# Optimization experiments

Hardware: AMD Instinct MI355X
Metric: run time of the kernel (lower is better)

The kernel has to match this reference:

```python
import jax, jax.numpy as jnp
import numpy as np
import math

B, N, E, D = 8, 2048, 2048, 128
MAX_K = 8
HYPER_DIM = 128
LN_EPS = 1e-5


def _sinusoidal_pe(max_pos, dim):
    pe = np.zeros((max_pos, dim), dtype=np.float32)
    position = np.arange(max_pos, dtype=np.float32)[:, None]
    div_term = np.exp(np.arange(0, dim, 2, dtype=np.float32) * (-math.log(10000.0) / dim))
    pe[:, 0::2] = np.sin(position * div_term)
    pe[:, 1::2] = np.cos(position * div_term)
    return jnp.asarray(pe)


def setup_inputs() -> dict:
    key = jax.random.key(0)
    ks = jax.random.split(key, 24)
    s = 0.05
    inp = {
        'x_v': jax.random.normal(ks[0], (B, N, D), jnp.float32),
        'x_e': jax.random.normal(ks[1], (B, E, D), jnp.float32),
        'incidence': (jax.random.uniform(ks[2], (B, N, E), jnp.float32) < 0.01).astype(jnp.float32),
        'suffix_normalizer': jax.random.uniform(ks[3], (B, N), jnp.float32) * 20.0,
        'edge_orders': 1 + jax.random.randint(ks[4], (B, E), 0, MAX_K),
        'node_mask': jax.random.randint(ks[5], (B, N), 0, 2) > 0,
        'edge_mask': jax.random.randint(ks[6], (B, E), 0, 2) > 0,
        'pe1_table': _sinusoidal_pe(MAX_K + 1, D),
        'pe2_table': _sinusoidal_pe(2, D),
        'bias_b': jax.random.uniform(ks[7], (1, D), jnp.float32, -1, 1) / math.sqrt(D),
    }
    i = 8
    for m in ('mlp1', 'mlp2', 'mlp3'):
        inp[m + '_W1'] = jax.random.normal(ks[i], (D, HYPER_DIM), jnp.float32) * s; i += 1
        inp[m + '_b1'] = jnp.zeros((HYPER_DIM,), jnp.float32)
        inp[m + '_W2'] = jax.random.normal(ks[i], (HYPER_DIM, D), jnp.float32) * s; i += 1
        inp[m + '_b2'] = jnp.zeros((D,), jnp.float32)
    for n in ('norm1', 'norm2', 'norm3'):
        inp[n + '_g'] = jnp.ones((D,), jnp.float32)
        inp[n + '_b'] = jnp.zeros((D,), jnp.float32)
    return inp


def _ln(x, g, b):
    mu = jnp.mean(x, axis=-1, keepdims=True)
    var = jnp.mean(jnp.square(x - mu), axis=-1, keepdims=True)
    return (x - mu) * jax.lax.rsqrt(var + LN_EPS) * g + b


def _mlp(x, W1, b1, W2, b2):
    return jax.nn.relu(x @ W1 + b1) @ W2 + b2


def reference(x_v, x_e, incidence, suffix_normalizer, edge_orders, node_mask, edge_mask,
              pe1_table, pe2_table, bias_b,
              mlp1_W1, mlp1_b1, mlp1_W2, mlp1_b2,
              mlp2_W1, mlp2_b1, mlp2_W2, mlp2_b2,
              mlp3_W1, mlp3_b1, mlp3_W2, mlp3_b2,
              norm1_g, norm1_b, norm2_g, norm2_b, norm3_g, norm3_b):
    nm = node_mask[..., None]  # [B,N,1]
    em = edge_mask[..., None]  # [B,E,1]
    x_v = jnp.where(nm, x_v, 0.0)
    x_e = jnp.where(em, x_e, 0.0)
    pe1_k1 = pe1_table[1][None, None, :]          # [1,1,D]
    pe1_k = pe1_table[edge_orders]                # [B,E,D]
    x_v = x_v + _mlp(_ln(x_v, norm1_g, norm1_b) + pe1_k1, mlp1_W1, mlp1_b1, mlp1_W2, mlp1_b2)
    x_e = x_e + _mlp(_ln(x_e, norm1_g, norm1_b) + pe1_k, mlp1_W1, mlp1_b1, mlp1_W2, mlp1_b2)
    x_v = jnp.where(nm, x_v, 0.0)
    x_e = jnp.where(em, x_e, 0.0)
    agg = jnp.einsum('bne,bed->bnd', incidence, x_e)
    x1 = x_v + agg / (1.0 + suffix_normalizer[..., None])
    pe2_s1 = pe2_table[1][None, None, :]
    x1 = x1 + _mlp(_ln(x1, norm2_g, norm2_b) + pe2_s1, mlp2_W1, mlp2_b1, mlp2_W2, mlp2_b2)
    x = jnp.where(nm, x1, 0.0)
    x = x + _mlp(_ln(x, norm3_g, norm3_b), mlp3_W1, mlp3_b1, mlp3_W2, mlp3_b2)
    x = x + bias_b
    x = jnp.where(nm, x, 0.0)
    return x
```

## Files before the change

### kernel.cpp

```cpp
#include <hip/hip_runtime.h>
#include <stdint.h>

#define BB 8
#define NN 2048
#define EE 2048
#define DD 128
#define RBP 132
#define NTHREADS 256
#define WMAT_U32 8192
#define LCAP 64

typedef __attribute__((ext_vector_type(8))) short bf16x8;
typedef __attribute__((ext_vector_type(4))) float f32x4;

__device__ inline unsigned bf16rne(float f) {
    unsigned u = __float_as_uint(f);
    return (u + 0x7fffu + ((u >> 16) & 1u)) >> 16;
}
__device__ inline float bf16lo(unsigned u) { return __uint_as_float(u << 16); }
__device__ inline float bf16hi(unsigned u) { return __uint_as_float(u & 0xffff0000u); }

#define SWZ(b) ((b) ^ ((((b) >> 8) & 7) << 4))

struct __align__(16) SmemK1 {
    float rowbuf[32][RBP];
    unsigned h[32 * 64];
    int rmask[32];
    int ords[32];
};

struct __align__(16) SmemK3 {
    float rowbuf[16][RBP];
    unsigned h[16 * 64];
    int rmask[16];
};

__device__ inline void load_rows32(SmemK1& s, const float* __restrict__ src) {
    int t = threadIdx.x;
    for (int idx = t; idx < 32 * 32; idx += NTHREADS) {
        int r = idx >> 5, c4 = (idx & 31) * 4;
        float4 v = *(const float4*)&src[r * DD + c4];
        *(float4*)&s.rowbuf[r][c4] = v;
    }
    __syncthreads();
    for (int idx = t; idx < 32 * 32; idx += NTHREADS) {
        int r = idx >> 5, c4 = (idx & 31) * 4;
        if (s.rmask[r] == 0) *(float4*)&s.rowbuf[r][c4] = make_float4(0.f, 0.f, 0.f, 0.f);
    }
    __syncthreads();
}

__device__ inline void ln32(SmemK1& s, const float* __restrict__ gw,
                            const float* __restrict__ bw,
                            const float* __restrict__ pe_base, bool per_row_pe) {
    int t = threadIdx.x;
    int gr = t >> 3, g = t & 7;
    int base = g * 16;
    float x[16];
    float4* xp = (float4*)x;
    xp[0] = *(const float4*)&s.rowbuf[gr][base + 0];
    xp[1] = *(const float4*)&s.rowbuf[gr][base + 4];
    xp[2] = *(const float4*)&s.rowbuf[gr][base + 8];
    xp[3] = *(const float4*)&s.rowbuf[gr][base + 12];
    float s1 = 0.f, s2 = 0.f;
    #pragma unroll
    for (int i = 0; i < 16; i++) { s1 += x[i]; s2 += x[i] * x[i]; }
    #pragma unroll
    for (int off = 1; off < 8; off <<= 1) {
        s1 += __shfl_xor(s1, off, 64);
        s2 += __shfl_xor(s2, off, 64);
    }
    float mu = s1 * (1.f / 128.f);
    float var = s2 * (1.f / 128.f) - mu * mu;
    float rstd = rsqrtf(var + 1e-5f);
    const float* pe = nullptr;
    if (pe_base) pe = per_row_pe ? (pe_base + (size_t)s.ords[gr] * DD) : pe_base;
    unsigned p[8];
    #pragma unroll
    for (int j = 0; j < 8; j++) {
        int k0 = base + 2 * j;
        float v0 = (x[2 * j] - mu) * rstd * gw[k0] + bw[k0];
        float v1 = (x[2 * j + 1] - mu) * rstd * gw[k0 + 1] + bw[k0 + 1];
        if (pe) { v0 += pe[k0]; v1 += pe[k0 + 1]; }
        p[j] = bf16rne(v0) | (bf16rne(v1) << 16);
    }
    char* hb = (char*)s.h;
    int byte0 = gr * 256 + g * 32;
    uint4 lo = make_uint4(p[0], p[1], p[2], p[3]);
    uint4 hi = make_uint4(p[4], p[5], p[6], p[7]);
    *(uint4*)(hb + SWZ(byte0)) = lo;
    *(uint4*)(hb + SWZ(byte0 + 16)) = hi;
    __syncthreads();
}

template <bool TO_H>
__device__ inline void mm32_f32w(SmemK1& s, const float* __restrict__ Wf,
                                 const float* __restrict__ bias) {
    int t = threadIdx.x;
    int w = t >> 6, l = t & 63;
    int lm = l & 15, lk = l >> 4;
    bf16x8 bfr[2][4];
    #pragma unroll
    for (int nbl = 0; nbl < 2; nbl++) {
        int n = w * 32 + nbl * 16 + lm;
        #pragma unroll
        for (int kb = 0; kb < 4; kb++) {
            int k0 = kb * 32 + lk * 8;
            unsigned pk[4];
            #pragma unroll
            for (int jp = 0; jp < 4; jp++) {
                float a = Wf[(size_t)(k0 + 2 * jp) * DD + n];
                float b = Wf[(size_t)(k0 + 2 * jp + 1) * DD + n];
                pk[jp] = bf16rne(a) | (bf16rne(b) << 16);
            }
            uint4 u = make_uint4(pk[0], pk[1], pk[2], pk[3]);
            bfr[nbl][kb] = *(bf16x8*)&u;
        }
    }
    const char* hb = (const char*)s.h;
    bf16x8 afr[2][4];
    #pragma unroll
    for (int mb = 0; mb < 2; mb++) {
        int row = mb * 16 + lm;
        #pragma unroll
        for (int kb = 0; kb < 4; kb++)
            afr[mb][kb] = *(const bf16x8*)(hb + SWZ(row * 256 + kb * 64 + lk * 16));
    }
    f32x4 acc[2][2];
    #pragma unroll
    for (int mb = 0; mb < 2; mb++)
        #pragma unroll
        for (int nbl = 0; nbl < 2; nbl++)
            acc[mb][nbl] = (f32x4){0.f, 0.f, 0.f, 0.f};
    #pragma unroll
    for (int kb = 0; kb < 4; kb++)
        #pragma unroll
        for (int mb = 0; mb < 2; mb++)
            #pragma unroll
            for (int nbl = 0; nbl < 2; nbl++)
                acc[mb][nbl] = __builtin_amdgcn_mfma_f32_16x16x32_bf16(
                    afr[mb][kb], bfr[nbl][kb], acc[mb][nbl], 0, 0, 0);
    float bcol0 = bias[w * 32 + lm];
    float bcol1 = bias[w * 32 + 16 + lm];
    __syncthreads();
    if (TO_H) {
        char* hw = (char*)s.h;
        #pragma unroll
        for (int mb = 0; mb < 2; mb++)
            #pragma unroll
            for (int nbl = 0; nbl < 2; nbl++) {
                int col = w * 32 + nbl * 16 + lm;
                float bc = nbl ? bcol1 : bcol0;
                #pragma unroll
                for (int j = 0; j < 4; j++) {
                    int row = mb * 16 + lk * 4 + j;
                    float v = fmaxf(acc[mb][nbl][j] + bc, 0.f);
                    *(unsigned short*)(hw + SWZ(row * 256 + col * 2)) =
                        (unsigned short)bf16rne(v);
                }
            }
    } else {
        #pragma unroll
        for (int mb = 0; mb < 2; mb++)
            #pragma unroll
            for (int nbl = 0; nbl < 2; nbl++) {
                int col = w * 32 + nbl * 16 + lm;
                float bc = nbl ? bcol1 : bcol0;
                #pragma unroll
                for (int j = 0; j < 4; j++) {
                    int row = mb * 16 + lk * 4 + j;
                    s.rowbuf[row][col] += acc[mb][nbl][j] + bc;
                }
            }
    }
    __syncthreads();
}

__device__ inline void ln16(SmemK3& s, const float* __restrict__ gw,
                            const float* __restrict__ bw,
                            const float* __restrict__ pe) {
    int t = threadIdx.x;
    int gr = t >> 4, g = t & 15;
    int base = g * 8;
    float x[8];
    float4* xp = (float4*)x;
    xp[0] = *(const float4*)&s.rowbuf[gr][base + 0];
    xp[1] = *(const float4*)&s.rowbuf[gr][base + 4];
    float s1 = 0.f, s2 = 0.f;
    #pragma unroll
    for (int i = 0; i < 8; i++) { s1 += x[i]; s2 += x[i] * x[i]; }
    #pragma unroll
    for (int off = 1; off < 16; off <<= 1) {
        s1 += __shfl_xor(s1, off, 64);
        s2 += __shfl_xor(s2, off, 64);
    }
    float mu = s1 * (1.f / 128.f);
    float var = s2 * (1.f / 128.f) - mu * mu;
    float rstd = rsqrtf(var + 1e-5f);
    unsigned p[4];
    #pragma unroll
    for (int j = 0; j < 4; j++) {
        int k0 = base + 2 * j;
        float v0 = (x[2 * j] - mu) * rstd * gw[k0] + bw[k0];
        float v1 = (x[2 * j + 1] - mu) * rstd * gw[k0 + 1] + bw[k0 + 1];
        if (pe) { v0 += pe[k0]; v1 += pe[k0 + 1]; }
        p[j] = bf16rne(v0) | (bf16rne(v1) << 16);
    }
    char* hb = (char*)s.h;
    uint4 q = make_uint4(p[0], p[1], p[2], p[3]);
    *(uint4*)(hb + SWZ(gr * 256 + g * 16)) = q;
    __syncthreads();
}

template <bool TO_H>
__device__ inline void mm16(SmemK3& s, const unsigned* __restrict__ WT,
                            const float* __restrict__ bias) {
    int t = threadIdx.x;
    int w = t >> 6, l = t & 63;
    int lm = l & 15, lk = l >> 4;
    bf16x8 bfr[2][4];
    const uint4* wt4 = (const uint4*)WT;
    #pragma unroll
    for (int nbl = 0; nbl < 2; nbl++) {
        int n = w * 32 + nbl * 16 + lm;
        #pragma unroll
        for (int kb = 0; kb < 4; kb++) {
            uint4 u = wt4[n * 16 + kb * 4 + lk];
            bfr[nbl][kb] = *(bf16x8*)&u;
        }
    }
    const char* hb = (const char*)s.h;
    bf16x8 afr[4];
    #pragma unroll
    for (int kb = 0; kb < 4; kb++)
        afr[kb] = *(const bf16x8*)(hb + SWZ(lm * 256 + kb * 64 + lk * 16));
    f32x4 acc[2];
    acc[0] = (f32x4){0.f, 0.f, 0.f, 0.f};
    acc[1] = (f32x4){0.f, 0.f, 0.f, 0.f};
    #pragma unroll
    for (int kb = 0; kb < 4; kb++)
        #pragma unroll
        for (int nbl = 0; nbl < 2; nbl++)
            acc[nbl] = __builtin_amdgcn_mfma_f32_16x16x32_bf16(
                afr[kb], bfr[nbl][kb], acc[nbl], 0, 0, 0);
    float bcol0 = bias[w * 32 + lm];
    float bcol1 = bias[w * 32 + 16 + lm];
    __syncthreads();
    if (TO_H) {
        char* hw = (char*)s.h;
        #pragma unroll
        for (int nbl = 0; nbl < 2; nbl++) {
            int col = w * 32 + nbl * 16 + lm;
            float bc = nbl ? bcol1 : bcol0;
            #pragma unroll
            for (int j = 0; j < 4; j++) {
                int row = lk * 4 + j;
                float v = fmaxf(acc[nbl][j] + bc, 0.f);
                *(unsigned short*)(hw + SWZ(row * 256 + col * 2)) =
                    (unsigned short)bf16rne(v);
            }
        }
    } else {
        #pragma unroll
        for (int nbl = 0; nbl < 2; nbl++) {
            int col = w * 32 + nbl * 16 + lm;
            float bc = nbl ? bcol1 : bcol0;
            #pragma unroll
            for (int j = 0; j < 4; j++) {
                int row = lk * 4 + j;
                s.rowbuf[row][col] += acc[nbl][j] + bc;
            }
        }
    }
    __syncthreads();
}

__global__ __launch_bounds__(NTHREADS) void k1_kernel(
    const float* __restrict__ x_e, const float* __restrict__ x_v,
    const int* __restrict__ emask, const int* __restrict__ nmask,
    const int* __restrict__ eord, const float* __restrict__ pe1,
    const float* __restrict__ n1g, const float* __restrict__ n1b,
    const float* __restrict__ W11, const float* __restrict__ b11,
    const float* __restrict__ W12, const float* __restrict__ b12,
    const float* __restrict__ W21, const float* __restrict__ W22,
    const float* __restrict__ W31, const float* __restrict__ W32,
    unsigned* __restrict__ WT, unsigned* __restrict__ e2pk,
    float* __restrict__ v2out) {
    __shared__ SmemK1 s;
    int bid = blockIdx.x;
    int t = threadIdx.x;
    int gtid = bid * NTHREADS + t;
    if (gtid < 4 * WMAT_U32) {
        int mat = gtid >> 13;
        int idx = gtid & (WMAT_U32 - 1);
        int n = idx >> 6, j = idx & 63;
        const float* W = mat == 0 ? W21 : mat == 1 ? W22 : mat == 2 ? W31 : W32;
        float a = W[(2 * j) * DD + n];
        float b = W[(2 * j + 1) * DD + n];
        WT[gtid] = bf16rne(a) | (bf16rne(b) << 16);
    }
    bool isEdge = bid < (BB * EE / 32);
    int mb = isEdge ? bid : bid - (BB * EE / 32);
    int bb = mb & 7;
    int r0 = (mb >> 3) * 32;
    int rowbase = bb * EE + r0;
    const int* mask = isEdge ? emask : nmask;
    if (t < 32) {
        s.rmask[t] = mask[rowbase + t];
        if (isEdge) {
            int o = eord[rowbase + t];
            s.ords[t] = o < 0 ? 0 : (o > 8 ? 8 : o);
        }
    }
    __syncthreads();
    load_rows32(s, (isEdge ? x_e : x_v) + (size_t)rowbase * DD);
    ln32(s, n1g, n1b, isEdge ? pe1 : (pe1 + DD), isEdge);
    mm32_f32w<true>(s, W11, b11);
    mm32_f32w<false>(s, W12, b12);
    if (isEdge) {
        unsigned* dst = e2pk + (size_t)rowbase * (DD / 2);
        for (int idx = t; idx < 32 * 16; idx += NTHREADS) {
            int r = idx >> 4, q = idx & 15;
            uint4 o = make_uint4(0u, 0u, 0u, 0u);
            if (s.rmask[r] != 0) {
                const float* rp = &s.rowbuf[r][q * 8];
                o.x = bf16rne(rp[0]) | (bf16rne(rp[1]) << 16);
                o.y = bf16rne(rp[2]) | (bf16rne(rp[3]) << 16);
                o.z = bf16rne(rp[4]) | (bf16rne(rp[5]) << 16);
                o.w = bf16rne(rp[6]) | (bf16rne(rp[7]) << 16);
            }
            *(uint4*)&dst[r * 64 + q * 4] = o;
        }
    } else {
        for (int idx = t; idx < 32 * 32; idx += NTHREADS) {
            int r = idx >> 5, c4 = (idx & 31) * 4;
            float4 v = make_float4(0.f, 0.f, 0.f, 0.f);
            if (s.rmask[r] != 0) v = *(const float4*)&s.rowbuf[r][c4];
            *(float4*)&v2out[(size_t)(rowbase + r) * DD + c4] = v;
        }
    }
}

__global__ __launch_bounds__(NTHREADS) void k2_kernel(
    const float* __restrict__ inc, const int* __restrict__ nmask,
    const float* __restrict__ sn, const unsigned* __restrict__ e2pk,
    float* __restrict__ agg) {
    __shared__ unsigned scw[4][64];
    int wib = threadIdx.x >> 6, l = threadIdx.x & 63;
    int grow = blockIdx.x * 4 + wib;
    if (grow >= BB * NN) return;
    if (nmask[grow] == 0) return;
    unsigned long long lmlt = (1ull << l) - 1ull;
    const float4* ir = (const float4*)(inc + (size_t)grow * EE);
    float4 v[8];
    #pragma unroll
    for (int i = 0; i < 8; i++) v[i] = ir[l + 64 * i];
    unsigned* sc = scw[wib];
    int total = 0;
    #pragma unroll
    for (int i = 0; i < 8; i++) {
        #pragma unroll
        for (int c = 0; c < 4; c++) {
            float a = (c == 0) ? v[i].x : (c == 1) ? v[i].y : (c == 2) ? v[i].z : v[i].w;
            bool nz = (a != 0.f);
            unsigned long long msk = __ballot(nz);
            if (nz) {
                int p = total + __popcll(msk & lmlt);
                if (p < LCAP) sc[p] = (unsigned)((l + 64 * i) * 4 + c);
            }
            total += __popcll(msk);
        }
    }
    if (total > LCAP) total = LCAP;
    asm volatile("s_waitcnt lgkmcnt(0)" ::: "memory");
    unsigned pk = (l < total) ? sc[l] : 0u;
    const unsigned* e2b = e2pk + (size_t)(grow >> 11) * (EE * (DD / 2));
    float ax = 0.f, ay = 0.f;
    for (int j0 = 0; j0 < total; j0 += 8) {
        int nn = total - j0;
        unsigned uv[8];
        #pragma unroll
        for (int u = 0; u < 8; u++) {
            unsigned e = __shfl(pk, j0 + u, 64);
            uv[u] = (u < nn) ? e2b[(size_t)e * 64 + l] : 0u;
        }
        #pragma unroll
        for (int u = 0; u < 8; u++) { ax += bf16lo(uv[u]); ay += bf16hi(uv[u]); }
    }
    float inv = 1.f / (1.f + sn[grow]);
    *(float2*)&agg[(size_t)grow * DD + 2 * l] = make_float2(ax * inv, ay * inv);
}

__global__ __launch_bounds__(NTHREADS) void k3_kernel(
    const float* __restrict__ v2, const int* __restrict__ nmask,
    const float* __restrict__ agg,
    const float* __restrict__ pe2, const float* __restrict__ biasb,
    const float* __restrict__ n2g, const float* __restrict__ n2b,
    const float* __restrict__ n3g, const float* __restrict__ n3b,
    const unsigned* __restrict__ WT,
    const float* __restrict__ b21, const float* __restrict__ b22,
    const float* __restrict__ b31, const float* __restrict__ b32,
    float* __restrict__ out) {
    __shared__ SmemK3 s;
    int bid = blockIdx.x;
    int bb = bid & 7;
    int n0 = (bid >> 3) * 16;
    int row0 = bb * NN + n0;
    int t = threadIdx.x;
    if (t < 16) s.rmask[t] = nmask[row0 + t];
    for (int idx = t; idx < 16 * 32; idx += NTHREADS) {
        int r = idx >> 5, c4 = (idx & 31) * 4;
        float4 v = *(const float4*)&v2[(size_t)(row0 + r) * DD + c4];
        *(float4*)&s.rowbuf[r][c4] = v;
    }
    __syncthreads();
    for (int idx = t; idx < 16 * 32; idx += NTHREADS) {
        int r = idx >> 5, c4 = (idx & 31) * 4;
        if (s.rmask[r] != 0) {
            float4 a = *(const float4*)&agg[(size_t)(row0 + r) * DD + c4];
            float4* rb = (float4*)&s.rowbuf[r][c4];
            float4 cur = *rb;
            cur.x += a.x; cur.y += a.y; cur.z += a.z; cur.w += a.w;
            *rb = cur;
        }
    }
    __syncthreads();
    ln16(s, n2g, n2b, pe2 + DD);
    mm16<true>(s, WT + 0 * WMAT_U32, b21);
    mm16<false>(s, WT + 1 * WMAT_U32, b22);
    ln16(s, n3g, n3b, nullptr);
    mm16<true>(s, WT + 2 * WMAT_U32, b31);
    mm16<false>(s, WT + 3 * WMAT_U32, b32);
    for (int idx = t; idx < 16 * 32; idx += NTHREADS) {
        int r = idx >> 5, c4 = (idx & 31) * 4;
        float4 v = make_float4(0.f, 0.f, 0.f, 0.f);
        if (s.rmask[r] != 0) {
            v = *(const float4*)&s.rowbuf[r][c4];
            float4 bbv = *(const float4*)&biasb[c4];
            v.x += bbv.x; v.y += bbv.y; v.z += bbv.z; v.w += bbv.w;
        }
        *(float4*)&out[(size_t)(row0 + r) * DD + c4] = v;
    }
}

extern "C" void kernel_launch(void* const* d_in, const int* in_sizes, int n_in,
                              void* d_out, int out_size, void* d_ws, size_t ws_size,
                              hipStream_t stream) {
    const float* x_v   = (const float*)d_in[0];
    const float* x_e   = (const float*)d_in[1];
    const float* inc   = (const float*)d_in[2];
    const float* sn    = (const float*)d_in[3];
    const int*   eord  = (const int*)d_in[4];
    const int*   nmask = (const int*)d_in[5];
    const int*   emask = (const int*)d_in[6];
    const float* pe1   = (const float*)d_in[7];
    const float* pe2   = (const float*)d_in[8];
    const float* biasb = (const float*)d_in[9];
    const float* W11   = (const float*)d_in[10];
    const float* b11   = (const float*)d_in[11];
    const float* W12   = (const float*)d_in[12];
    const float* b12   = (const float*)d_in[13];
    const float* W21   = (const float*)d_in[14];
    const float* b21   = (const float*)d_in[15];
    const float* W22   = (const float*)d_in[16];
    const float* b22   = (const float*)d_in[17];
    const float* W31   = (const float*)d_in[18];
    const float* b31   = (const float*)d_in[19];
    const float* W32   = (const float*)d_in[20];
    const float* b32   = (const float*)d_in[21];
    const float* n1g   = (const float*)d_in[22];
    const float* n1b   = (const float*)d_in[23];
    const float* n2g   = (const float*)d_in[24];
    const float* n2b   = (const float*)d_in[25];
    const float* n3g   = (const float*)d_in[26];
    const float* n3b   = (const float*)d_in[27];

    unsigned* e2pk = (unsigned*)d_ws;
    unsigned* WT   = e2pk + (size_t)BB * EE * (DD / 2);
    float*    agg  = (float*)(WT + 4 * WMAT_U32);
    float*    out  = (float*)d_out;

    dim3 blk(NTHREADS);
    k1_kernel<<<dim3(2 * BB * EE / 32), blk, 0, stream>>>(
        x_e, x_v, emask, nmask, eord, pe1,
        n1g, n1b, W11, b11, W12, b12, W21, W22, W31, W32,
        WT, e2pk, out);
    k2_kernel<<<dim3(BB * NN / 4), blk, 0, stream>>>(
        inc, nmask, sn, e2pk, agg);
    k3_kernel<<<dim3(BB * NN / 16), blk, 0, stream>>>(
        out, nmask, agg, pe2, biasb,
        n2g, n2b, n3g, n3b,
        WT, b21, b22, b31, b32, out);
}
```

Baseline: 64.19 us.

## Move node-side MLP1 tiles into the scan/gather kernel to balance work

The node-row MLP1 tiles move out of the first kernel and into the incidence-scan/gather kernel as extra blocks appended after the scan blocks. The first kernel now only processes edge rows and the weight transposes. The aim is to shorten the critical first kernel and overlap the compute-bound node MLP with the memory-bound incidence scan. In exchange, the second kernel now uses the larger SmemK1 shared allocation for every block, which may lower occupancy for the scan blocks.

New measurement: 86.51 us. +34.8%, slower.

```diff
diff --git a/kernel.cpp b/kernel.cpp
--- a/kernel.cpp
+++ b/kernel.cpp
@@ -8,6 +8,7 @@
 #define RBP 132
 #define NTHREADS 256
 #define WMAT_U32 8192
+#define SCANGB 4096
 #define LCAP 64
 
 typedef __attribute__((ext_vector_type(8))) short bf16x8;
@@ -176,135 +177,16 @@
     __syncthreads();
 }
 
-__device__ inline void ln16(SmemK3& s, const float* __restrict__ gw,
-                            const float* __restrict__ bw,
-                            const float* __restrict__ pe) {
-    int t = threadIdx.x;
-    int gr = t >> 4, g = t & 15;
-    int base = g * 8;
-    float x[8];
-    float4* xp = (float4*)x;
-    xp[0] = *(const float4*)&s.rowbuf[gr][base + 0];
-    xp[1] = *(const float4*)&s.rowbuf[gr][base + 4];
-    float s1 = 0.f, s2 = 0.f;
-    #pragma unroll
-    for (int i = 0; i < 8; i++) { s1 += x[i]; s2 += x[i] * x[i]; }
-    #pragma unroll
-    for (int off = 1; off < 16; off <<= 1) {
-        s1 += __shfl_xor(s1, off, 64);
-        s2 += __shfl_xor(s2, off, 64);
-    }
-    float mu = s1 * (1.f / 128.f);
-    float var = s2 * (1.f / 128.f) - mu * mu;
-    float rstd = rsqrtf(var + 1e-5f);
-    unsigned p[4];
-    #pragma unroll
-    for (int j = 0; j < 4; j++) {
-        int k0 = base + 2 * j;
-        float v0 = (x[2 * j] - mu) * rstd * gw[k0] + bw[k0];
-        float v1 = (x[2 * j + 1] - mu) * rstd * gw[k0 + 1] + bw[k0 + 1];
-        if (pe) { v0 += pe[k0]; v1 += pe[k0 + 1]; }
-        p[j] = bf16rne(v0) | (bf16rne(v1) << 16);
-    }
-    char* hb = (char*)s.h;
-    uint4 q = make_uint4(p[0], p[1], p[2], p[3]);
-    *(uint4*)(hb + SWZ(gr * 256 + g * 16)) = q;
-    __syncthreads();
-}
-
-template <bool TO_H>
-__device__ inline void mm16(SmemK3& s, const unsigned* __restrict__ WT,
-                            const float* __restrict__ bias) {
-    int t = threadIdx.x;
-    int w = t >> 6, l = t & 63;
-    int lm = l & 15, lk = l >> 4;
-    bf16x8 bfr[2][4];
-    const uint4* wt4 = (const uint4*)WT;
-    #pragma unroll
-    for (int nbl = 0; nbl < 2; nbl++) {
-        int n = w * 32 + nbl * 16 + lm;
-        #pragma unroll
-        for (int kb = 0; kb < 4; kb++) {
-            uint4 u = wt4[n * 16 + kb * 4 + lk];
-            bfr[nbl][kb] = *(bf16x8*)&u;
-        }
-    }
-    const char* hb = (const char*)s.h;
-    bf16x8 afr[4];
-    #pragma unroll
-    for (int kb = 0; kb < 4; kb++)
-        afr[kb] = *(const bf16x8*)(hb + SWZ(lm * 256 + kb * 64 + lk * 16));
-    f32x4 acc[2];
-    acc[0] = (f32x4){0.f, 0.f, 0.f, 0.f};
-    acc[1] = (f32x4){0.f, 0.f, 0.f, 0.f};
-    #pragma unroll
-    for (int kb = 0; kb < 4; kb++)
-        #pragma unroll
-        for (int nbl = 0; nbl < 2; nbl++)
-            acc[nbl] = __builtin_amdgcn_mfma_f32_16x16x32_bf16(
-                afr[kb], bfr[nbl][kb], acc[nbl], 0, 0, 0);
-    float bcol0 = bias[w * 32 + lm];
-    float bcol1 = bias[w * 32 + 16 + lm];
-    __syncthreads();
-    if (TO_H) {
-        char* hw = (char*)s.h;
-        #pragma unroll
-        for (int nbl = 0; nbl < 2; nbl++) {
-            int col = w * 32 + nbl * 16 + lm;
-            float bc = nbl ? bcol1 : bcol0;
-            #pragma unroll
-            for (int j = 0; j < 4; j++) {
-                int row = lk * 4 + j;
-                float v = fmaxf(acc[nbl][j] + bc, 0.f);
-                *(unsigned short*)(hw + SWZ(row * 256 + col * 2)) =
-                    (unsigned short)bf16rne(v);
-            }
-        }
-    } else {
-        #pragma unroll
-        for (int nbl = 0; nbl < 2; nbl++) {
-            int col = w * 32 + nbl * 16 + lm;
-            float bc = nbl ? bcol1 : bcol0;
-            #pragma unroll
-            for (int j = 0; j < 4; j++) {
-                int row = lk * 4 + j;
-                s.rowbuf[row][col] += acc[nbl][j] + bc;
-            }
-        }
-    }
-    __syncthreads();
-}
-
-__global__ __launch_bounds__(NTHREADS) void k1_kernel(
-    const float* __restrict__ x_e, const float* __restrict__ x_v,
-    const int* __restrict__ emask, const int* __restrict__ nmask,
-    const int* __restrict__ eord, const float* __restrict__ pe1,
-    const float* __restrict__ n1g, const float* __restrict__ n1b,
-    const float* __restrict__ W11, const float* __restrict__ b11,
-    const float* __restrict__ W12, const float* __restrict__ b12,
-    const float* __restrict__ W21, const float* __restrict__ W22,
-    const float* __restrict__ W31, const float* __restrict__ W32,
-    unsigned* __restrict__ WT, unsigned* __restrict__ e2pk,
-    float* __restrict__ v2out) {
-    __shared__ SmemK1 s;
-    int bid = blockIdx.x;
-    int t = threadIdx.x;
-    int gtid = bid * NTHREADS + t;
-    if (gtid < 4 * WMAT_U32) {
-        int mat = gtid >> 13;
-        int idx = gtid & (WMAT_U32 - 1);
-        int n = idx >> 6, j = idx & 63;
-        const float* W = mat == 0 ? W21 : mat == 1 ? W22 : mat == 2 ? W31 : W32;
-        float a = W[(2 * j) * DD + n];
-        float b = W[(2 * j + 1) * DD + n];
-        WT[gtid] = bf16rne(a) | (bf16rne(b) << 16);
-    }
-    bool isEdge = bid < (BB * EE / 32);
-    int mb = isEdge ? bid : bid - (BB * EE / 32);
-    int bb = mb & 7;
-    int r0 = (mb >> 3) * 32;
-    int rowbase = bb * EE + r0;
-    const int* mask = isEdge ? emask : nmask;
+__device__ inline void mlp1_tile(SmemK1& s, bool isEdge, int rowbase,
+                                 const float* __restrict__ xsrc,
+                                 const int* __restrict__ mask,
+                                 const int* __restrict__ eord,
+                                 const float* __restrict__ pe1,
+                                 const float* __restrict__ n1g, const float* __restrict__ n1b,
+                                 const float* __restrict__ W11, const float* __restrict__ b11,
+                                 const float* __restrict__ W12, const float* __restrict__ b12,
+                                 unsigned* __restrict__ e2pk, float* __restrict__ v2out) {
+    int t = threadIdx.x;
     if (t < 32) {
         s.rmask[t] = mask[rowbase + t];
         if (isEdge) {
@@ -313,7 +195,7 @@
         }
     }
     __syncthreads();
-    load_rows32(s, (isEdge ? x_e : x_v) + (size_t)rowbase * DD);
+    load_rows32(s, xsrc + (size_t)rowbase * DD);
     ln32(s, n1g, n1b, isEdge ? pe1 : (pe1 + DD), isEdge);
     mm32_f32w<true>(s, W11, b11);
     mm32_f32w<false>(s, W12, b12);
@@ -341,54 +223,197 @@
     }
 }
 
+__global__ __launch_bounds__(NTHREADS) void k1_kernel(
+    const float* __restrict__ x_e, const int* __restrict__ emask,
+    const int* __restrict__ eord, const float* __restrict__ pe1,
+    const float* __restrict__ n1g, const float* __restrict__ n1b,
+    const float* __restrict__ W11, const float* __restrict__ b11,
+    const float* __restrict__ W12, const float* __restrict__ b12,
+    const float* __restrict__ W21, const float* __restrict__ W22,
+    const float* __restrict__ W31, const float* __restrict__ W32,
+    unsigned* __restrict__ WT, unsigned* __restrict__ e2pk) {
+    __shared__ SmemK1 s;
+    int bid = blockIdx.x;
+    int t = threadIdx.x;
+    int gtid = bid * NTHREADS + t;
+    if (gtid < 4 * WMAT_U32) {
+        int mat = gtid >> 13;
+        int idx = gtid & (WMAT_U32 - 1);
+        int n = idx >> 6, j = idx & 63;
+        const float* W = mat == 0 ? W21 : mat == 1 ? W22 : mat == 2 ? W31 : W32;
+        float a = W[(2 * j) * DD + n];
+        float b = W[(2 * j + 1) * DD + n];
+        WT[gtid] = bf16rne(a) | (bf16rne(b) << 16);
+    }
+    int bb = bid & 7;
+    int r0 = (bid >> 3) * 32;
+    int rowbase = bb * EE + r0;
+    mlp1_tile(s, true, rowbase, x_e, emask, eord, pe1,
+              n1g, n1b, W11, b11, W12, b12, e2pk, nullptr);
+}
+
 __global__ __launch_bounds__(NTHREADS) void k2_kernel(
     const float* __restrict__ inc, const int* __restrict__ nmask,
     const float* __restrict__ sn, const unsigned* __restrict__ e2pk,
-    float* __restrict__ agg) {
-    __shared__ unsigned scw[4][64];
-    int wib = threadIdx.x >> 6, l = threadIdx.x & 63;
-    int grow = blockIdx.x * 4 + wib;
-    if (grow >= BB * NN) return;
-    if (nmask[grow] == 0) return;
-    unsigned long long lmlt = (1ull << l) - 1ull;
-    const float4* ir = (const float4*)(inc + (size_t)grow * EE);
-    float4 v[8];
-    #pragma unroll
-    for (int i = 0; i < 8; i++) v[i] = ir[l + 64 * i];
-    unsigned* sc = scw[wib];
-    int total = 0;
-    #pragma unroll
-    for (int i = 0; i < 8; i++) {
-        #pragma unroll
-        for (int c = 0; c < 4; c++) {
-            float a = (c == 0) ? v[i].x : (c == 1) ? v[i].y : (c == 2) ? v[i].z : v[i].w;
-            bool nz = (a != 0.f);
-            unsigned long long msk = __ballot(nz);
-            if (nz) {
-                int p = total + __popcll(msk & lmlt);
-                if (p < LCAP) sc[p] = (unsigned)((l + 64 * i) * 4 + c);
-            }
-            total += __popcll(msk);
-        }
-    }
-    if (total > LCAP) total = LCAP;
-    asm volatile("s_waitcnt lgkmcnt(0)" ::: "memory");
-    unsigned pk = (l < total) ? sc[l] : 0u;
-    const unsigned* e2b = e2pk + (size_t)(grow >> 11) * (EE * (DD / 2));
-    float ax = 0.f, ay = 0.f;
-    for (int j0 = 0; j0 < total; j0 += 8) {
-        int nn = total - j0;
-        unsigned uv[8];
-        #pragma unroll
-        for (int u = 0; u < 8; u++) {
-            unsigned e = __shfl(pk, j0 + u, 64);
-            uv[u] = (u < nn) ? e2b[(size_t)e * 64 + l] : 0u;
-        }
-        #pragma unroll
-        for (int u = 0; u < 8; u++) { ax += bf16lo(uv[u]); ay += bf16hi(uv[u]); }
-    }
-    float inv = 1.f / (1.f + sn[grow]);
-    *(float2*)&agg[(size_t)grow * DD + 2 * l] = make_float2(ax * inv, ay * inv);
+    float* __restrict__ agg,
+    const float* __restrict__ x_v, const float* __restrict__ pe1,
+    const float* __restrict__ n1g, const float* __restrict__ n1b,
+    const float* __restrict__ W11, const float* __restrict__ b11,
+    const float* __restrict__ W12, const float* __restrict__ b12,
+    float* __restrict__ v2out) {
+    __shared__ SmemK1 s;
+    int bid = blockIdx.x;
+    int t = threadIdx.x;
+    if (bid < SCANGB) {
+        int wib = t >> 6, l = t & 63;
+        int grow = bid * 4 + wib;
+        if (nmask[grow] == 0) return;
+        unsigned long long lmlt = (1ull << l) - 1ull;
+        const float4* ir = (const float4*)(inc + (size_t)grow * EE);
+        float4 v[8];
+        #pragma unroll
+        for (int i = 0; i < 8; i++) v[i] = ir[l + 64 * i];
+        unsigned* sc = &s.h[wib * 64];
+        int total = 0;
+        #pragma unroll
+        for (int i = 0; i < 8; i++) {
+            #pragma unroll
+            for (int c = 0; c < 4; c++) {
+                float a = (c == 0) ? v[i].x : (c == 1) ? v[i].y : (c == 2) ? v[i].z : v[i].w;
+                bool nz = (a != 0.f);
+                unsigned long long msk = __ballot(nz);
+                if (nz) {
+                    int p = total + __popcll(msk & lmlt);
+                    if (p < LCAP) sc[p] = (unsigned)((l + 64 * i) * 4 + c);
+                }
+                total += __popcll(msk);
+            }
+        }
+        if (total > LCAP) total = LCAP;
+        asm volatile("s_waitcnt lgkmcnt(0)" ::: "memory");
+        unsigned pk = (l < total) ? sc[l] : 0u;
+        const unsigned* e2b = e2pk + (size_t)(grow >> 11) * (EE * (DD / 2));
+        float ax = 0.f, ay = 0.f;
+        for (int j0 = 0; j0 < total; j0 += 8) {
+            int nn = total - j0;
+            unsigned uv[8];
+            #pragma unroll
+            for (int u = 0; u < 8; u++) {
+                unsigned e = __shfl(pk, j0 + u, 64);
+                uv[u] = (u < nn) ? e2b[(size_t)e * 64 + l] : 0u;
+            }
+            #pragma unroll
+            for (int u = 0; u < 8; u++) { ax += bf16lo(uv[u]); ay += bf16hi(uv[u]); }
+        }
+        float inv = 1.f / (1.f + sn[grow]);
+        *(float2*)&agg[(size_t)grow * DD + 2 * l] = make_float2(ax * inv, ay * inv);
+        return;
+    }
+    int mb = bid - SCANGB;
+    int bb = mb & 7;
+    int r0 = (mb >> 3) * 32;
+    int rowbase = bb * NN + r0;
+    mlp1_tile(s, false, rowbase, x_v, nmask, nullptr, pe1,
+              n1g, n1b, W11, b11, W12, b12, nullptr, v2out);
+}
+
+__device__ inline void ln16(SmemK3& s, const float* __restrict__ gw,
+                            const float* __restrict__ bw,
+                            const float* __restrict__ pe) {
+    int t = threadIdx.x;
+    int gr = t >> 4, g = t & 15;
+    int base = g * 8;
+    float x[8];
+    float4* xp = (float4*)x;
+    xp[0] = *(const float4*)&s.rowbuf[gr][base + 0];
+    xp[1] = *(const float4*)&s.rowbuf[gr][base + 4];
+    float s1 = 0.f, s2 = 0.f;
+    #pragma unroll
+    for (int i = 0; i < 8; i++) { s1 += x[i]; s2 += x[i] * x[i]; }
+    #pragma unroll
+    for (int off = 1; off < 16; off <<= 1) {
+        s1 += __shfl_xor(s1, off, 64);
+        s2 += __shfl_xor(s2, off, 64);
+    }
+    float mu = s1 * (1.f / 128.f);
+    float var = s2 * (1.f / 128.f) - mu * mu;
+    float rstd = rsqrtf(var + 1e-5f);
+    unsigned p[4];
+    #pragma unroll
+    for (int j = 0; j < 4; j++) {
+        int k0 = base + 2 * j;
+        float v0 = (x[2 * j] - mu) * rstd * gw[k0] + bw[k0];
+        float v1 = (x[2 * j + 1] - mu) * rstd * gw[k0 + 1] + bw[k0 + 1];
+        if (pe) { v0 += pe[k0]; v1 += pe[k0 + 1]; }
+        p[j] = bf16rne(v0) | (bf16rne(v1) << 16);
+    }
+    char* hb = (char*)s.h;
+    uint4 q = make_uint4(p[0], p[1], p[2], p[3]);
+    *(uint4*)(hb + SWZ(gr * 256 + g * 16)) = q;
+    __syncthreads();
+}
+
+template <bool TO_H>
+__device__ inline void mm16(SmemK3& s, const unsigned* __restrict__ WT,
+                            const float* __restrict__ bias) {
+    int t = threadIdx.x;
+    int w = t >> 6, l = t & 63;
+    int lm = l & 15, lk = l >> 4;
+    bf16x8 bfr[2][4];
+    const uint4* wt4 = (const uint4*)WT;
+    #pragma unroll
+    for (int nbl = 0; nbl < 2; nbl++) {
+        int n = w * 32 + nbl * 16 + lm;
+        #pragma unroll
+        for (int kb = 0; kb < 4; kb++) {
+            uint4 u = wt4[n * 16 + kb * 4 + lk];
+            bfr[nbl][kb] = *(bf16x8*)&u;
+        }
+    }
+    const char* hb = (const char*)s.h;
+    bf16x8 afr[4];
+    #pragma unroll
+    for (int kb = 0; kb < 4; kb++)
+        afr[kb] = *(const bf16x8*)(hb + SWZ(lm * 256 + kb * 64 + lk * 16));
+    f32x4 acc[2];
+    acc[0] = (f32x4){0.f, 0.f, 0.f, 0.f};
+    acc[1] = (f32x4){0.f, 0.f, 0.f, 0.f};
+    #pragma unroll
+    for (int kb = 0; kb < 4; kb++)
+        #pragma unroll
+        for (int nbl = 0; nbl < 2; nbl++)
+            acc[nbl] = __builtin_amdgcn_mfma_f32_16x16x32_bf16(
+                afr[kb], bfr[nbl][kb], acc[nbl], 0, 0, 0);
+    float bcol0 = bias[w * 32 + lm];
+    float bcol1 = bias[w * 32 + 16 + lm];
+    __syncthreads();
+    if (TO_H) {
+        char* hw = (char*)s.h;
+        #pragma unroll
+        for (int nbl = 0; nbl < 2; nbl++) {
+            int col = w * 32 + nbl * 16 + lm;
+            float bc = nbl ? bcol1 : bcol0;
+            #pragma unroll
+            for (int j = 0; j < 4; j++) {
+                int row = lk * 4 + j;
+                float v = fmaxf(acc[nbl][j] + bc, 0.f);
+                *(unsigned short*)(hw + SWZ(row * 256 + col * 2)) =
+                    (unsigned short)bf16rne(v);
+            }
+        }
+    } else {
+        #pragma unroll
+        for (int nbl = 0; nbl < 2; nbl++) {
+            int col = w * 32 + nbl * 16 + lm;
+            float bc = nbl ? bcol1 : bcol0;
+            #pragma unroll
+            for (int j = 0; j < 4; j++) {
+                int row = lk * 4 + j;
+                s.rowbuf[row][col] += acc[nbl][j] + bc;
+            }
+        }
+    }
+    __syncthreads();
 }
 
 __global__ __launch_bounds__(NTHREADS) void k3_kernel(
@@ -481,12 +506,12 @@
     float*    out  = (float*)d_out;
 
     dim3 blk(NTHREADS);
-    k1_kernel<<<dim3(2 * BB * EE / 32), blk, 0, stream>>>(
-        x_e, x_v, emask, nmask, eord, pe1,
-        n1g, n1b, W11, b11, W12, b12, W21, W22, W31, W32,
-        WT, e2pk, out);
-    k2_kernel<<<dim3(BB * NN / 4), blk, 0, stream>>>(
-        inc, nmask, sn, e2pk, agg);
+    k1_kernel<<<dim3(BB * EE / 32), blk, 0, stream>>>(
+        x_e, emask, eord, pe1, n1g, n1b, W11, b11, W12, b12,
+        W21, W22, W31, W32, WT, e2pk);
+    k2_kernel<<<dim3(SCANGB + BB * NN / 32), blk, 0, stream>>>(
+        inc, nmask, sn, e2pk, agg,
+        x_v, pe1, n1g, n1b, W11, b11, W12, b12, out);
     k3_kernel<<<dim3(BB * NN / 16), blk, 0, stream>>>(
         out, nmask, agg, pe2, biasb,
         n2g, n2b, n3g, n3b,
```
